# Performance work log

Measured on AMD Instinct MI355X. Metric: run time of the kernel, lower is better.

Reference implementation:

```python
import jax, jax.numpy as jnp
import numpy as np

N = 50000
NEG_SLOPE = 0.2


def leaky_relu(x, slope=NEG_SLOPE):
    return jnp.where(x >= 0, x, slope * x)


def gat_conv(x, edge_index, W, a_src, a_dst, bias):
    """PyG GATConv, heads=1, add_self_loops=True.
    x: [N, Fin], edge_index: [2, E] (row 0 = source j, row 1 = target i),
    W: [Fin, Fout], a_src/a_dst: [Fout], bias: [Fout].
    """
    n = x.shape[0]
    # add self loops
    loops = jnp.arange(n, dtype=edge_index.dtype)
    src = jnp.concatenate([edge_index[0], loops])
    dst = jnp.concatenate([edge_index[1], loops])

    xw = x @ W                       # [N, Fout]
    alpha_src = xw @ a_src           # [N]
    alpha_dst = xw @ a_dst           # [N]

    e = leaky_relu(alpha_src[src] + alpha_dst[dst])   # [E+N]
    # segment softmax over edges sharing the same target node
    m = jax.ops.segment_max(e, dst, num_segments=n)   # [N]
    ex = jnp.exp(e - m[dst])
    denom = jax.ops.segment_sum(ex, dst, num_segments=n)  # [N] (>0 via self loops)
    att = ex / denom[dst]                              # [E+N]

    msgs = att[:, None] * xw[src]                      # [E+N, Fout]
    out = jax.ops.segment_sum(msgs, dst, num_segments=n)
    return out + bias


def setup_inputs() -> dict:
    key = jax.random.key(0)
    ks = jax.random.split(key, 12)
    E = 800000
    Fin, H, Fout = 128, 256, 128
    x = jax.random.normal(ks[0], (N, Fin), dtype=jnp.float32)
    edge_index = jax.random.randint(ks[1], (2, E), 0, N, dtype=jnp.int64)
    s = 0.1
    W1 = jax.random.normal(ks[2], (Fin, H), dtype=jnp.float32) * s
    a1_src = jax.random.normal(ks[3], (H,), dtype=jnp.float32) * s
    a1_dst = jax.random.normal(ks[4], (H,), dtype=jnp.float32) * s
    b1 = jax.random.normal(ks[5], (H,), dtype=jnp.float32) * s
    W2 = jax.random.normal(ks[6], (H, Fout), dtype=jnp.float32) * s
    a2_src = jax.random.normal(ks[7], (Fout,), dtype=jnp.float32) * s
    a2_dst = jax.random.normal(ks[8], (Fout,), dtype=jnp.float32) * s
    b2 = jax.random.normal(ks[9], (Fout,), dtype=jnp.float32) * s
    return {"x": x, "edge_index": edge_index, "W1": W1, "a1_src": a1_src,
            "a1_dst": a1_dst, "b1": b1, "W2": W2, "a2_src": a2_src,
            "a2_dst": a2_dst, "b2": b2}


def reference(x, edge_index, W1, a1_src, a1_dst, b1, W2, a2_src, a2_dst, b2):
    h = jax.nn.relu(gat_conv(x, edge_index, W1, a1_src, a1_dst, b1))
    return gat_conv(h, edge_index, W2, a2_src, a2_dst, b2)
```

## Files before the change

### kernel.cpp

```cpp
#include <hip/hip_runtime.h>
#include <hip/hip_bf16.h>

typedef __attribute__((ext_vector_type(8))) short short8;
typedef __attribute__((ext_vector_type(4))) float floatx4;

#define CAP 8192
#define BIN_CH 2048
#define NPB 32

__device__ __forceinline__ float read_f(const void* p, long long i, int fp32m) {
  return fp32m ? ((const float*)p)[i] : (float)((const __hip_bfloat16*)p)[i];
}
__device__ __forceinline__ float bf2f(unsigned short u) {
  return __uint_as_float((unsigned)u << 16);
}
__device__ __forceinline__ unsigned short f2bf(float f) {
  const unsigned u = __float_as_uint(f);
  return (unsigned short)((u + 0x7fffu + ((u >> 16) & 1u)) >> 16);
}

__device__ __forceinline__ void pack_one(const void* W, unsigned short* Wp, int i,
                                         int K, int NOUT, int m) {
  const int k = i / NOUT, n = i - k * NOUT;
  const int ct = n >> 4, c = n & 15, ks = k >> 5, quad = (k >> 3) & 3, j = k & 7;
  Wp[(((ct * (K / 32) + ks) * 4 + quad) * 16 + c) * 8 + j] = f2bf(read_f(W, i, m));
}

__global__ __launch_bounds__(256) void prep_k(const void* __restrict__ x,
                                              const void* __restrict__ ei,
                                              const void* __restrict__ W1,
                                              const void* __restrict__ a1s,
                                              const void* __restrict__ a1d,
                                              const void* __restrict__ b1,
                                              const void* __restrict__ W2,
                                              const void* __restrict__ a2s,
                                              const void* __restrict__ a2d,
                                              const void* __restrict__ b2,
                                              unsigned short* __restrict__ Wp1,
                                              unsigned short* __restrict__ Wp2,
                                              float* __restrict__ w_as1, float* __restrict__ w_ad1,
                                              float* __restrict__ v_a2s, float* __restrict__ v_a2d,
                                              float* __restrict__ v_b1,  float* __restrict__ v_b2,
                                              int* __restrict__ bkcnt,
                                              int* __restrict__ flags) {
  __shared__ int fl_s[2];
  const int t = threadIdx.x, b = blockIdx.x;
  if (t < 64) {
    const unsigned short w = ((const unsigned short*)x)[t * 2];
    const int ef = (w >> 7) & 0xff;
    const bool bf_ok = (ef >= 90 && ef <= 140);
    const unsigned hi = ((const unsigned*)ei)[t * 2 + 1];
    const unsigned long long bm = __ballot(bf_ok);
    const unsigned long long zm = __ballot(hi == 0u);
    if (t == 0) {
      fl_s[0] = (bm == ~0ull) ? 0 : 1;
      fl_s[1] = (zm == ~0ull) ? 1 : 0;
      if (b == 0) { flags[0] = fl_s[0]; flags[1] = fl_s[1]; }
    }
  }
  __syncthreads();
  const int m = fl_s[0];

  if (b < 128) {
    pack_one(W1, Wp1, b * 256 + t, 128, 256, m);
  } else if (b < 256) {
    pack_one(W2, Wp2, (b - 128) * 256 + t, 256, 128, m);
  } else if (b == 256) {
    if (t < 128) {
      float sa = 0.f, sb = 0.f;
      for (int j = 0; j < 256; ++j) {
        const float w = read_f(W1, (long long)t * 256 + j, m);
        sa = fmaf(w, read_f(a1s, j, m), sa);
        sb = fmaf(w, read_f(a1d, j, m), sb);
      }
      w_as1[t] = sa;
      w_ad1[t] = sb;
    }
  } else if (b == 257) {
    if (t < 128) v_a2s[t] = read_f(a2s, t, m);
    else         v_a2d[t - 128] = read_f(a2d, t - 128, m);
  } else if (b == 258) {
    v_b1[t] = read_f(b1, t, m);
  } else {
    if (t < 128) v_b2[t] = read_f(b2, t, m);
    bkcnt[t] = 0;
  }
}

__device__ __forceinline__ void edge_sd(const void* ei, int e, int E, int i64m, int n,
                                        int& s, int& d) {
  if (e < E) {
    if (i64m) { s = (int)((const long long*)ei)[e]; d = (int)((const long long*)ei)[E + e]; }
    else      { s = ((const int*)ei)[e];            d = ((const int*)ei)[E + e]; }
  } else { s = d = e - E; }
  s = min(max(s, 0), n - 1);
  d = min(max(d, 0), n - 1);
}

__global__ __launch_bounds__(256) void front2_k(const void* __restrict__ x,
                                                const void* __restrict__ ei,
                                                const float* __restrict__ w_as1,
                                                const float* __restrict__ w_ad1,
                                                unsigned short* __restrict__ xb,
                                                float* __restrict__ as_, float* __restrict__ ad_,
                                                unsigned* __restrict__ bpool,
                                                int* __restrict__ bkcnt,
                                                int n, int E, int EN, int nbc) {
  __shared__ int fl_s[2];
  __shared__ unsigned stage[BIN_CH];
  __shared__ unsigned daddr[BIN_CH];
  __shared__ int shA[256], shB[256], shC[256], shD[256];
  __shared__ int vtot_s;
  const int t = threadIdx.x, b = blockIdx.x;

  if (t < 64) {
    const unsigned short w = ((const unsigned short*)x)[t * 2];
    const int ef = (w >> 7) & 0xff;
    const bool bf_ok = (ef >= 90 && ef <= 140);
    const unsigned hi = ((const unsigned*)ei)[t * 2 + 1];
    const unsigned long long bm = __ballot(bf_ok);
    const unsigned long long zm = __ballot(hi == 0u);
    if (t == 0) {
      fl_s[0] = (bm == ~0ull) ? 0 : 1;
      fl_s[1] = (zm == ~0ull) ? 1 : 0;
    }
  }
  __syncthreads();
  const int m = fl_s[0], i64m = fl_s[1];

  if (b < nbc) {
    const int gid = b * 256 + t;
    const int node = gid >> 6, lane = gid & 63;
    if (node >= n) return;
    const long long base = (long long)node * 128 + lane * 2;
    const float v0 = read_f(x, base, m), v1 = read_f(x, base + 1, m);
    ushort2 q;
    q.x = f2bf(v0); q.y = f2bf(v1);
    *(ushort2*)(xb + base) = q;
    float s1 = fmaf(v0, w_as1[lane * 2], v1 * w_as1[lane * 2 + 1]);
    float s2 = fmaf(v0, w_ad1[lane * 2], v1 * w_ad1[lane * 2 + 1]);
    for (int off = 32; off; off >>= 1) {
      s1 += __shfl_down(s1, off);
      s2 += __shfl_down(s2, off);
    }
    if (lane == 0) { as_[node] = s1; ad_[node] = s2; }
  } else {
    const int c0 = (b - nbc) * BIN_CH;
    int* bcnt_s = shA; int* boff_s = shB; int* gbase_s = shC; int* sd = shD;
    bcnt_s[t] = 0;
    __syncthreads();

    unsigned val[BIN_CH / 256];
    int buk[BIN_CH / 256];
#pragma unroll
    for (int i = 0; i < BIN_CH / 256; ++i) {
      const int e = c0 + i * 256 + t;
      if (e < EN) {
        int s, d;
        edge_sd(ei, e, E, i64m, n, s, d);
        buk[i] = d >> 8;
        val[i] = (unsigned)s | ((unsigned)(d & 255) << 16);
        atomicAdd(&bcnt_s[buk[i]], 1);
      } else buk[i] = -1;
    }
    __syncthreads();

    const int c = bcnt_s[t];
    sd[t] = c;
    __syncthreads();
    for (int off = 1; off < 256; off <<= 1) {
      const int v = (t >= off) ? sd[t - off] : 0;
      __syncthreads();
      sd[t] += v;
      __syncthreads();
    }
    boff_s[t] = sd[t] - c;
    if (t == 255) vtot_s = sd[255];
    gbase_s[t] = (c > 0) ? atomicAdd(&bkcnt[t], c) : 0;
    bcnt_s[t] = 0;
    __syncthreads();

#pragma unroll
    for (int i = 0; i < BIN_CH / 256; ++i) {
      if (buk[i] >= 0) {
        const int lp = atomicAdd(&bcnt_s[buk[i]], 1);
        const int si = boff_s[buk[i]] + lp;
        stage[si] = val[i];
        const int gp = gbase_s[buk[i]] + lp;
        daddr[si] = (gp < CAP) ? (unsigned)(buk[i] * CAP + gp) : 0xFFFFFFFFu;
      }
    }
    __syncthreads();

    const int vt = vtot_s;
    for (int idx = t; idx < vt; idx += 256)
      if (daddr[idx] != 0xFFFFFFFFu) bpool[daddr[idx]] = stage[idx];
  }
}

__global__ __launch_bounds__(256) void bucket_csr_k(const unsigned* __restrict__ bpool,
                                                    const int* __restrict__ bkcnt,
                                                    unsigned short* __restrict__ csrc,
                                                    int* __restrict__ start_g,
                                                    int* __restrict__ deg_g, int n) {
  __shared__ int deg_s[256], cur_s[256], sd[256];
  const int t = threadIdx.x, b = blockIdx.x;
  int cnt = bkcnt[b];
  if (cnt > CAP) cnt = CAP;
  deg_s[t] = 0;
  __syncthreads();
  for (int idx = t; idx < cnt; idx += 256) {
    const unsigned v = bpool[b * CAP + idx];
    atomicAdd(&deg_s[(v >> 16) & 255], 1);
  }
  __syncthreads();
  const int dg = deg_s[t];
  sd[t] = dg;
  __syncthreads();
  for (int off = 1; off < 256; off <<= 1) {
    const int v = (t >= off) ? sd[t - off] : 0;
    __syncthreads();
    sd[t] += v;
    __syncthreads();
  }
  const int excl = sd[t] - dg;
  const int node = b * 256 + t;
  if (node < n) { start_g[node] = b * CAP + excl; deg_g[node] = dg; }
  cur_s[t] = excl;
  __syncthreads();
  for (int idx = t; idx < cnt; idx += 256) {
    const unsigned v = bpool[b * CAP + idx];
    const int p = atomicAdd(&cur_s[(v >> 16) & 255], 1);
    csrc[b * CAP + p] = (unsigned short)(v & 0xFFFFu);
  }
}

__device__ __forceinline__ void agg_node(const int start, const int end,
                                         const unsigned short* __restrict__ csrc,
                                         const float* __restrict__ as_, const float adv,
                                         const unsigned short* __restrict__ xw,
                                         const int lane, float* acc) {
  const int slot = lane >> 4, col = lane & 15;
  float dsum = 0.f;
#pragma unroll
  for (int c = 0; c < 8; ++c) acc[c] = 0.f;

  for (int base = start; base < end; base += 64) {
    const int idx = base + lane;
    int s_pre = 0;
    float w_pre = 0.f;
    if (idx < end) {
      s_pre = (int)csrc[idx];
      float v = as_[s_pre] + adv;
      v = (v >= 0.f) ? v : 0.2f * v;
      w_pre = __expf(fminf(v, 60.f));
    }
    dsum += w_pre;
    const int cnt = min(64, end - base);
    for (int j = 0; j < cnt; j += 8) {
      const int jj0 = j + slot, jj1 = j + 4 + slot;
      int s0 = __shfl(s_pre, jj0);
      float w0 = __shfl(w_pre, jj0);
      int s1 = __shfl(s_pre, jj1);
      float w1 = __shfl(w_pre, jj1);
      const bool ok0 = (jj0 < cnt), ok1 = (jj1 < cnt);
      s0 = ok0 ? s0 : 0; w0 = ok0 ? w0 : 0.f;
      s1 = ok1 ? s1 : 0; w1 = ok1 ? w1 : 0.f;
      const short8 q0 = *(const short8*)(xw + (size_t)s0 * 128 + col * 8);
      const short8 q1 = *(const short8*)(xw + (size_t)s1 * 128 + col * 8);
#pragma unroll
      for (int c = 0; c < 8; ++c) {
        acc[c] = fmaf(w0, bf2f((unsigned short)q0[c]), acc[c]);
        acc[c] = fmaf(w1, bf2f((unsigned short)q1[c]), acc[c]);
      }
    }
  }
  for (int off = 32; off; off >>= 1) dsum += __shfl_down(dsum, off);
  dsum = __shfl(dsum, 0);
  const float r = 1.f / fmaxf(dsum, 1e-30f);
#pragma unroll
  for (int c = 0; c < 8; ++c) {
    acc[c] += __shfl_xor(acc[c], 16);
    acc[c] += __shfl_xor(acc[c], 32);
    acc[c] *= r;
  }
}

#define LSTR 136
#define HSTR 264
__global__ __launch_bounds__(1024) void agg_gemm12_k(const int* __restrict__ start_g,
                                                     const int* __restrict__ deg_g,
                                                     const unsigned short* __restrict__ csrc,
                                                     const float* __restrict__ as_,
                                                     const float* __restrict__ ad_,
                                                     const unsigned short* __restrict__ xb,
                                                     const unsigned short* __restrict__ Wp1,
                                                     const unsigned short* __restrict__ Wp2,
                                                     const float* __restrict__ v_b1,
                                                     const float* __restrict__ v_a2s,
                                                     const float* __restrict__ v_a2d,
                                                     unsigned short* __restrict__ xw2,
                                                     float* __restrict__ as2,
                                                     float* __restrict__ ad2, int n) {
  __shared__ unsigned short lds[NPB * LSTR];
  __shared__ unsigned short hs[NPB * HSTR];
  __shared__ float al_s[NPB], al_d[NPB];
  const int wv = threadIdx.x >> 6, lane = threadIdx.x & 63;
  const int slot = lane >> 4, col = lane & 15;
  const int node0 = blockIdx.x * NPB;

#pragma unroll
  for (int k = 0; k < 2; ++k) {
    const int rv = wv + 16 * k;
    const int node = node0 + rv;
    float acc[8];
    if (node < n) {
      const int start = start_g[node];
      agg_node(start, start + deg_g[node], csrc, as_, ad_[node], xb, lane, acc);
    } else {
#pragma unroll
      for (int c = 0; c < 8; ++c) acc[c] = 0.f;
    }
    if (slot == 0) {
      short8 q;
#pragma unroll
      for (int c = 0; c < 8; ++c) q[c] = (short)f2bf(acc[c]);
      *(short8*)&lds[rv * LSTR + col * 8] = q;
    }
  }
  if (threadIdx.x < NPB) { al_s[threadIdx.x] = 0.f; al_d[threadIdx.x] = 0.f; }
  __syncthreads();

  const int quad = slot, c = col;
  short8 bf1[4];
#pragma unroll
  for (int ks = 0; ks < 4; ++ks)
    bf1[ks] = *(const short8*)(Wp1 + (size_t)((wv * 4 + ks) * 64 + lane) * 8);
  const float bv = v_b1[wv * 16 + c];
#pragma unroll
  for (int rt = 0; rt < 2; ++rt) {
    floatx4 g = {0.f, 0.f, 0.f, 0.f};
#pragma unroll
    for (int ks = 0; ks < 4; ++ks) {
      const short8 af = *(const short8*)&lds[(rt * 16 + c) * LSTR + ks * 32 + quad * 8];
      g = __builtin_amdgcn_mfma_f32_16x16x32_bf16(af, bf1[ks], g, 0, 0, 0);
    }
#pragma unroll
    for (int r = 0; r < 4; ++r) {
      const float v = g[r] + bv;
      hs[(rt * 16 + quad * 4 + r) * HSTR + wv * 16 + c] = f2bf(v > 0.f ? v : 0.f);
    }
  }
  __syncthreads();

  const int ct = wv & 7, rt2 = wv >> 3;
  short8 bf2[8];
#pragma unroll
  for (int ks = 0; ks < 8; ++ks)
    bf2[ks] = *(const short8*)(Wp2 + (size_t)((ct * 8 + ks) * 64 + lane) * 8);
  floatx4 a2 = {0.f, 0.f, 0.f, 0.f};
#pragma unroll
  for (int ks = 0; ks < 8; ++ks) {
    const short8 af = *(const short8*)&hs[(rt2 * 16 + c) * HSTR + ks * 32 + quad * 8];
    a2 = __builtin_amdgcn_mfma_f32_16x16x32_bf16(af, bf2[ks], a2, 0, 0, 0);
  }
  const float asv = v_a2s[ct * 16 + c], adv = v_a2d[ct * 16 + c];
  float pa_s[4], pa_d[4];
#pragma unroll
  for (int r = 0; r < 4; ++r) {
    pa_s[r] = a2[r] * asv;
    pa_d[r] = a2[r] * adv;
    const int rr = node0 + rt2 * 16 + quad * 4 + r;
    if (rr < n) xw2[(size_t)rr * 128 + ct * 16 + c] = f2bf(a2[r]);
  }
  for (int off = 1; off < 16; off <<= 1) {
#pragma unroll
    for (int r = 0; r < 4; ++r) {
      pa_s[r] += __shfl_xor(pa_s[r], off);
      pa_d[r] += __shfl_xor(pa_d[r], off);
    }
  }
  if (c == 0) {
#pragma unroll
    for (int r = 0; r < 4; ++r) {
      atomicAdd(&al_s[rt2 * 16 + quad * 4 + r], pa_s[r]);
      atomicAdd(&al_d[rt2 * 16 + quad * 4 + r], pa_d[r]);
    }
  }
  __syncthreads();
  if (threadIdx.x < NPB) {
    const int rr = node0 + threadIdx.x;
    if (rr < n) { as2[rr] = al_s[threadIdx.x]; ad2[rr] = al_d[threadIdx.x]; }
  }
}

__global__ __launch_bounds__(256) void agg_out_k(const int* __restrict__ start_g,
                                                 const int* __restrict__ deg_g,
                                                 const unsigned short* __restrict__ csrc,
                                                 const float* __restrict__ as_,
                                                 const float* __restrict__ ad_,
                                                 const unsigned short* __restrict__ xw,
                                                 const float* __restrict__ bias,
                                                 void* __restrict__ outp, int n,
                                                 const int* __restrict__ flags) {
  const int gid = blockIdx.x * 256 + threadIdx.x;
  const int node = gid >> 6, lane = gid & 63;
  if (node >= n) return;
  const int slot = lane >> 4, col = lane & 15;
  const int start = start_g[node];
  float acc[8];
  agg_node(start, start + deg_g[node], csrc, as_, ad_[node], xw, lane, acc);
  if (slot == 0) {
    const int c0 = col * 8;
    if (flags[0]) {
      float* o = (float*)outp + (size_t)node * 128 + c0;
      floatx4 q0, q1;
#pragma unroll
      for (int c = 0; c < 4; ++c) {
        q0[c] = acc[c] + bias[c0 + c];
        q1[c] = acc[c + 4] + bias[c0 + 4 + c];
      }
      *(floatx4*)o = q0;
      *(floatx4*)(o + 4) = q1;
    } else {
      short8 q;
#pragma unroll
      for (int c = 0; c < 8; ++c) q[c] = (short)f2bf(acc[c] + bias[c0 + c]);
      *(short8*)((unsigned short*)outp + (size_t)node * 128 + c0) = q;
    }
  }
}

extern "C" void kernel_launch(void* const* d_in, const int* in_sizes, int n_in,
                              void* d_out, int out_size, void* d_ws, size_t ws_size,
                              hipStream_t stream) {
  const void* x   = d_in[0];
  const void* ei  = d_in[1];
  const void* W1  = d_in[2];
  const void* a1s = d_in[3];
  const void* a1d = d_in[4];
  const void* b1  = d_in[5];
  const void* W2  = d_in[6];
  const void* a2s = d_in[7];
  const void* a2d = d_in[8];
  const void* b2  = d_in[9];

  const int N  = in_sizes[0] / 128;
  const int E  = in_sizes[1] / 2;
  const int EN = E + N;
  const int NBUK = (N + 255) / 256;

  unsigned short* B1 = (unsigned short*)d_ws;
  unsigned short* H  = B1 + (size_t)N * 128;
  unsigned short* xw2 = H;
  float* as2 = (float*)(H + (size_t)N * 128);
  float* ad2 = as2 + N;
  float* as_   = (float*)(H + (size_t)N * 256);
  float* ad_   = as_ + N;
  int*   start_g = (int*)(ad_ + N);
  int*   deg_g   = start_g + N;
  int*   bkcnt   = deg_g + N;
  unsigned* bpool = (unsigned*)(bkcnt + 256);
  unsigned short* csrc = (unsigned short*)(bpool + (size_t)NBUK * CAP);
  unsigned short* Wp1 = csrc + (size_t)NBUK * CAP;
  unsigned short* Wp2 = Wp1 + 128 * 256;
  float* vecs  = (float*)(Wp2 + 256 * 128);
  int*   flags = (int*)(vecs + 1152);
  float* w_as1 = vecs,        *w_ad1 = vecs + 128;
  float* v_a2s = vecs + 256,  *v_a2d = vecs + 384;
  float* v_b1  = vecs + 512,  *v_b2  = vecs + 768;

  const int NB = (N * 64 + 255) / 256;
  const int BB = (EN + BIN_CH - 1) / BIN_CH;
  const int AG = (N + NPB - 1) / NPB;

  prep_k<<<260, 256, 0, stream>>>(x, ei, W1, a1s, a1d, b1, W2, a2s, a2d, b2,
                                  Wp1, Wp2, w_as1, w_ad1, v_a2s, v_a2d, v_b1, v_b2,
                                  bkcnt, flags);

  front2_k<<<NB + BB, 256, 0, stream>>>(x, ei, w_as1, w_ad1, B1, as_, ad_,
                                        bpool, bkcnt, N, E, EN, NB);

  bucket_csr_k<<<NBUK, 256, 0, stream>>>(bpool, bkcnt, csrc, start_g, deg_g, N);

  agg_gemm12_k<<<AG, 1024, 0, stream>>>(start_g, deg_g, csrc, as_, ad_, B1, Wp1, Wp2,
                                        v_b1, v_a2s, v_a2d, xw2, as2, ad2, N);

  agg_out_k<<<NB, 256, 0, stream>>>(start_g, deg_g, csrc, as2, ad2, xw2, v_b2, d_out, N, flags);
}
```

Before: 254.5 us.

## Shrink aggregation blocks to 16 nodes with 4 waves and rebalance GEMM tiling

The fused aggregation+two-GEMM kernel moves from 1024-thread blocks of 32 nodes to 256-thread blocks of 16 nodes. Each wave now aggregates 4 nodes and computes 4 (then 2) output column tiles, with the A fragment reused across tiles and B loaded from global per tile. The output aggregation kernel likewise processes 4 nodes per wave in 16-node blocks, and the CSR bucket kernel is widened to 1024 threads. The goal is better occupancy and load balance on skewed-degree nodes. The cost is that each block rereads the full weight matrices for only 16 rows.

```diff
diff --git a/kernel.cpp b/kernel.cpp
--- a/kernel.cpp
+++ b/kernel.cpp
@@ -6,7 +6,7 @@
 
 #define CAP 8192
 #define BIN_CH 2048
-#define NPB 32
+#define NPB 16
 
 __device__ __forceinline__ float read_f(const void* p, long long i, int fp32m) {
   return fp32m ? ((const float*)p)[i] : (float)((const __hip_bfloat16*)p)[i];
@@ -198,37 +198,39 @@
   }
 }
 
-__global__ __launch_bounds__(256) void bucket_csr_k(const unsigned* __restrict__ bpool,
-                                                    const int* __restrict__ bkcnt,
-                                                    unsigned short* __restrict__ csrc,
-                                                    int* __restrict__ start_g,
-                                                    int* __restrict__ deg_g, int n) {
+__global__ __launch_bounds__(1024) void bucket_csr_k(const unsigned* __restrict__ bpool,
+                                                     const int* __restrict__ bkcnt,
+                                                     unsigned short* __restrict__ csrc,
+                                                     int* __restrict__ start_g,
+                                                     int* __restrict__ deg_g, int n) {
   __shared__ int deg_s[256], cur_s[256], sd[256];
   const int t = threadIdx.x, b = blockIdx.x;
   int cnt = bkcnt[b];
   if (cnt > CAP) cnt = CAP;
-  deg_s[t] = 0;
-  __syncthreads();
-  for (int idx = t; idx < cnt; idx += 256) {
+  if (t < 256) deg_s[t] = 0;
+  __syncthreads();
+  for (int idx = t; idx < cnt; idx += 1024) {
     const unsigned v = bpool[b * CAP + idx];
     atomicAdd(&deg_s[(v >> 16) & 255], 1);
   }
   __syncthreads();
-  const int dg = deg_s[t];
-  sd[t] = dg;
+  const int dg = (t < 256) ? deg_s[t] : 0;
+  if (t < 256) sd[t] = dg;
   __syncthreads();
   for (int off = 1; off < 256; off <<= 1) {
-    const int v = (t >= off) ? sd[t - off] : 0;
-    __syncthreads();
-    sd[t] += v;
-    __syncthreads();
-  }
-  const int excl = sd[t] - dg;
-  const int node = b * 256 + t;
-  if (node < n) { start_g[node] = b * CAP + excl; deg_g[node] = dg; }
-  cur_s[t] = excl;
-  __syncthreads();
-  for (int idx = t; idx < cnt; idx += 256) {
+    const int v = (t < 256 && t >= off) ? sd[t - off] : 0;
+    __syncthreads();
+    if (t < 256) sd[t] += v;
+    __syncthreads();
+  }
+  if (t < 256) {
+    const int excl = sd[t] - dg;
+    const int node = b * 256 + t;
+    if (node < n) { start_g[node] = b * CAP + excl; deg_g[node] = dg; }
+    cur_s[t] = excl;
+  }
+  __syncthreads();
+  for (int idx = t; idx < cnt; idx += 1024) {
     const unsigned v = bpool[b * CAP + idx];
     const int p = atomicAdd(&cur_s[(v >> 16) & 255], 1);
     csrc[b * CAP + p] = (unsigned short)(v & 0xFFFFu);
@@ -288,20 +290,20 @@
 
 #define LSTR 136
 #define HSTR 264
-__global__ __launch_bounds__(1024) void agg_gemm12_k(const int* __restrict__ start_g,
-                                                     const int* __restrict__ deg_g,
-                                                     const unsigned short* __restrict__ csrc,
-                                                     const float* __restrict__ as_,
-                                                     const float* __restrict__ ad_,
-                                                     const unsigned short* __restrict__ xb,
-                                                     const unsigned short* __restrict__ Wp1,
-                                                     const unsigned short* __restrict__ Wp2,
-                                                     const float* __restrict__ v_b1,
-                                                     const float* __restrict__ v_a2s,
-                                                     const float* __restrict__ v_a2d,
-                                                     unsigned short* __restrict__ xw2,
-                                                     float* __restrict__ as2,
-                                                     float* __restrict__ ad2, int n) {
+__global__ __launch_bounds__(256, 8) void agg_gemm12_k(const int* __restrict__ start_g,
+                                                       const int* __restrict__ deg_g,
+                                                       const unsigned short* __restrict__ csrc,
+                                                       const float* __restrict__ as_,
+                                                       const float* __restrict__ ad_,
+                                                       const unsigned short* __restrict__ xb,
+                                                       const unsigned short* __restrict__ Wp1,
+                                                       const unsigned short* __restrict__ Wp2,
+                                                       const float* __restrict__ v_b1,
+                                                       const float* __restrict__ v_a2s,
+                                                       const float* __restrict__ v_a2d,
+                                                       unsigned short* __restrict__ xw2,
+                                                       float* __restrict__ as2,
+                                                       float* __restrict__ ad2, int n) {
   __shared__ unsigned short lds[NPB * LSTR];
   __shared__ unsigned short hs[NPB * HSTR];
   __shared__ float al_s[NPB], al_d[NPB];
@@ -309,9 +311,8 @@
   const int slot = lane >> 4, col = lane & 15;
   const int node0 = blockIdx.x * NPB;
 
-#pragma unroll
-  for (int k = 0; k < 2; ++k) {
-    const int rv = wv + 16 * k;
+  for (int k = 0; k < 4; ++k) {
+    const int rv = wv * 4 + k;
     const int node = node0 + rv;
     float acc[8];
     if (node < n) {
@@ -332,59 +333,60 @@
   __syncthreads();
 
   const int quad = slot, c = col;
-  short8 bf1[4];
+  short8 af1[4];
 #pragma unroll
   for (int ks = 0; ks < 4; ++ks)
-    bf1[ks] = *(const short8*)(Wp1 + (size_t)((wv * 4 + ks) * 64 + lane) * 8);
-  const float bv = v_b1[wv * 16 + c];
-#pragma unroll
-  for (int rt = 0; rt < 2; ++rt) {
+    af1[ks] = *(const short8*)&lds[c * LSTR + ks * 32 + quad * 8];
+#pragma unroll
+  for (int j = 0; j < 4; ++j) {
+    const int ct = wv * 4 + j;
     floatx4 g = {0.f, 0.f, 0.f, 0.f};
 #pragma unroll
     for (int ks = 0; ks < 4; ++ks) {
-      const short8 af = *(const short8*)&lds[(rt * 16 + c) * LSTR + ks * 32 + quad * 8];
-      g = __builtin_amdgcn_mfma_f32_16x16x32_bf16(af, bf1[ks], g, 0, 0, 0);
-    }
+      const short8 bf = *(const short8*)(Wp1 + (size_t)((ct * 4 + ks) * 64 + lane) * 8);
+      g = __builtin_amdgcn_mfma_f32_16x16x32_bf16(af1[ks], bf, g, 0, 0, 0);
+    }
+    const float bv = v_b1[ct * 16 + c];
 #pragma unroll
     for (int r = 0; r < 4; ++r) {
       const float v = g[r] + bv;
-      hs[(rt * 16 + quad * 4 + r) * HSTR + wv * 16 + c] = f2bf(v > 0.f ? v : 0.f);
-    }
-  }
-  __syncthreads();
-
-  const int ct = wv & 7, rt2 = wv >> 3;
-  short8 bf2[8];
-#pragma unroll
-  for (int ks = 0; ks < 8; ++ks)
-    bf2[ks] = *(const short8*)(Wp2 + (size_t)((ct * 8 + ks) * 64 + lane) * 8);
-  floatx4 a2 = {0.f, 0.f, 0.f, 0.f};
-#pragma unroll
-  for (int ks = 0; ks < 8; ++ks) {
-    const short8 af = *(const short8*)&hs[(rt2 * 16 + c) * HSTR + ks * 32 + quad * 8];
-    a2 = __builtin_amdgcn_mfma_f32_16x16x32_bf16(af, bf2[ks], a2, 0, 0, 0);
-  }
-  const float asv = v_a2s[ct * 16 + c], adv = v_a2d[ct * 16 + c];
-  float pa_s[4], pa_d[4];
-#pragma unroll
-  for (int r = 0; r < 4; ++r) {
-    pa_s[r] = a2[r] * asv;
-    pa_d[r] = a2[r] * adv;
-    const int rr = node0 + rt2 * 16 + quad * 4 + r;
-    if (rr < n) xw2[(size_t)rr * 128 + ct * 16 + c] = f2bf(a2[r]);
-  }
-  for (int off = 1; off < 16; off <<= 1) {
+      hs[(quad * 4 + r) * HSTR + ct * 16 + c] = f2bf(v > 0.f ? v : 0.f);
+    }
+  }
+  __syncthreads();
+
+#pragma unroll
+  for (int j2 = 0; j2 < 2; ++j2) {
+    const int ct = wv * 2 + j2;
+    floatx4 a2 = {0.f, 0.f, 0.f, 0.f};
+#pragma unroll
+    for (int ks = 0; ks < 8; ++ks) {
+      const short8 af = *(const short8*)&hs[c * HSTR + ks * 32 + quad * 8];
+      const short8 bf = *(const short8*)(Wp2 + (size_t)((ct * 8 + ks) * 64 + lane) * 8);
+      a2 = __builtin_amdgcn_mfma_f32_16x16x32_bf16(af, bf, a2, 0, 0, 0);
+    }
+    const float asv = v_a2s[ct * 16 + c], adv = v_a2d[ct * 16 + c];
+    float pa_s[4], pa_d[4];
 #pragma unroll
     for (int r = 0; r < 4; ++r) {
-      pa_s[r] += __shfl_xor(pa_s[r], off);
-      pa_d[r] += __shfl_xor(pa_d[r], off);
-    }
-  }
-  if (c == 0) {
-#pragma unroll
-    for (int r = 0; r < 4; ++r) {
-      atomicAdd(&al_s[rt2 * 16 + quad * 4 + r], pa_s[r]);
-      atomicAdd(&al_d[rt2 * 16 + quad * 4 + r], pa_d[r]);
+      pa_s[r] = a2[r] * asv;
+      pa_d[r] = a2[r] * adv;
+      const int rr = node0 + quad * 4 + r;
+      if (rr < n) xw2[(size_t)rr * 128 + ct * 16 + c] = f2bf(a2[r]);
+    }
+    for (int off = 1; off < 16; off <<= 1) {
+#pragma unroll
+      for (int r = 0; r < 4; ++r) {
+        pa_s[r] += __shfl_xor(pa_s[r], off);
+        pa_d[r] += __shfl_xor(pa_d[r], off);
+      }
+    }
+    if (c == 0) {
+#pragma unroll
+      for (int r = 0; r < 4; ++r) {
+        atomicAdd(&al_s[quad * 4 + r], pa_s[r]);
+        atomicAdd(&al_d[quad * 4 + r], pa_d[r]);
+      }
     }
   }
   __syncthreads();
@@ -394,39 +396,43 @@
   }
 }
 
-__global__ __launch_bounds__(256) void agg_out_k(const int* __restrict__ start_g,
-                                                 const int* __restrict__ deg_g,
-                                                 const unsigned short* __restrict__ csrc,
-                                                 const float* __restrict__ as_,
-                                                 const float* __restrict__ ad_,
-                                                 const unsigned short* __restrict__ xw,
-                                                 const float* __restrict__ bias,
-                                                 void* __restrict__ outp, int n,
-                                                 const int* __restrict__ flags) {
-  const int gid = blockIdx.x * 256 + threadIdx.x;
-  const int node = gid >> 6, lane = gid & 63;
-  if (node >= n) return;
+__global__ __launch_bounds__(256, 8) void agg_out_k(const int* __restrict__ start_g,
+                                                    const int* __restrict__ deg_g,
+                                                    const unsigned short* __restrict__ csrc,
+                                                    const float* __restrict__ as_,
+                                                    const float* __restrict__ ad_,
+                                                    const unsigned short* __restrict__ xw,
+                                                    const float* __restrict__ bias,
+                                                    void* __restrict__ outp, int n,
+                                                    const int* __restrict__ flags) {
+  const int wv = threadIdx.x >> 6, lane = threadIdx.x & 63;
   const int slot = lane >> 4, col = lane & 15;
-  const int start = start_g[node];
-  float acc[8];
-  agg_node(start, start + deg_g[node], csrc, as_, ad_[node], xw, lane, acc);
-  if (slot == 0) {
-    const int c0 = col * 8;
-    if (flags[0]) {
-      float* o = (float*)outp + (size_t)node * 128 + c0;
-      floatx4 q0, q1;
-#pragma unroll
-      for (int c = 0; c < 4; ++c) {
-        q0[c] = acc[c] + bias[c0 + c];
-        q1[c] = acc[c + 4] + bias[c0 + 4 + c];
-      }
-      *(floatx4*)o = q0;
-      *(floatx4*)(o + 4) = q1;
-    } else {
-      short8 q;
-#pragma unroll
-      for (int c = 0; c < 8; ++c) q[c] = (short)f2bf(acc[c] + bias[c0 + c]);
-      *(short8*)((unsigned short*)outp + (size_t)node * 128 + c0) = q;
+  const int node0 = blockIdx.x * 16;
+  const int fm = flags[0];
+  for (int k = 0; k < 4; ++k) {
+    const int node = node0 + wv * 4 + k;
+    if (node >= n) continue;
+    const int start = start_g[node];
+    float acc[8];
+    agg_node(start, start + deg_g[node], csrc, as_, ad_[node], xw, lane, acc);
+    if (slot == 0) {
+      const int c0 = col * 8;
+      if (fm) {
+        float* o = (float*)outp + (size_t)node * 128 + c0;
+        floatx4 q0, q1;
+#pragma unroll
+        for (int c = 0; c < 4; ++c) {
+          q0[c] = acc[c] + bias[c0 + c];
+          q1[c] = acc[c + 4] + bias[c0 + 4 + c];
+        }
+        *(floatx4*)o = q0;
+        *(floatx4*)(o + 4) = q1;
+      } else {
+        short8 q;
+#pragma unroll
+        for (int c = 0; c < 8; ++c) q[c] = (short)f2bf(acc[c] + bias[c0 + c]);
+        *(short8*)((unsigned short*)outp + (size_t)node * 128 + c0) = q;
+      }
     }
   }
 }
@@ -481,10 +487,10 @@
   front2_k<<<NB + BB, 256, 0, stream>>>(x, ei, w_as1, w_ad1, B1, as_, ad_,
                                         bpool, bkcnt, N, E, EN, NB);
 
-  bucket_csr_k<<<NBUK, 256, 0, stream>>>(bpool, bkcnt, csrc, start_g, deg_g, N);
-
-  agg_gemm12_k<<<AG, 1024, 0, stream>>>(start_g, deg_g, csrc, as_, ad_, B1, Wp1, Wp2,
-                                        v_b1, v_a2s, v_a2d, xw2, as2, ad2, N);
-
-  agg_out_k<<<NB, 256, 0, stream>>>(start_g, deg_g, csrc, as2, ad2, xw2, v_b2, d_out, N, flags);
-}
+  bucket_csr_k<<<NBUK, 1024, 0, stream>>>(bpool, bkcnt, csrc, start_g, deg_g, N);
+
+  agg_gemm12_k<<<AG, 256, 0, stream>>>(start_g, deg_g, csrc, as_, ad_, B1, Wp1, Wp2,
+                                       v_b1, v_a2s, v_a2d, xw2, as2, ad2, N);
+
+  agg_out_k<<<AG, 256, 0, stream>>>(start_g, deg_g, csrc, as2, ad2, xw2, v_b2, d_out, N, flags);
+}
```

Result: faster. 247.5 us (-2.8%).
